# Performance work log

Hardware: AMD Instinct MI355X
Metric: run time of the kernel (lower is better)

Reference implementation:

```python
import jax, jax.numpy as jnp
import numpy as np

IN_FEATURES = 128
OUT_FEATURES = 1
N_NODES = 100000
N_EDGES = 640000


def setup_inputs() -> dict:
    key = jax.random.key(0)
    k1, k2, k3, k4, k5 = jax.random.split(key, 5)
    inp = jax.random.normal(k1, (N_NODES, IN_FEATURES), dtype=jnp.float32)
    edge_src = jax.random.randint(k2, (N_EDGES,), 0, N_NODES, dtype=jnp.int64)
    edge_trg = jax.random.randint(k3, (N_EDGES,), 0, N_NODES, dtype=jnp.int64)
    # Linear(2*in_features, out_features) with xavier_uniform weight init
    fan_in, fan_out = 2 * IN_FEATURES, OUT_FEATURES
    limit = float(np.sqrt(6.0 / (fan_in + fan_out)))
    W = jax.random.uniform(k4, (OUT_FEATURES, 2 * IN_FEATURES), dtype=jnp.float32,
                           minval=-limit, maxval=limit)
    b_lim = 1.0 / float(np.sqrt(fan_in))
    b = jax.random.uniform(k5, (OUT_FEATURES,), dtype=jnp.float32,
                           minval=-b_lim, maxval=b_lim)
    return {"input": inp, "edge_src_nodes": edge_src, "edge_trg_nodes": edge_trg,
            "W": W, "b": b}


def reference(input, W, b, edge_src_nodes, edge_trg_nodes):
    x = input.reshape(-1, input.shape[-1])          # [N, d]
    src = x[edge_src_nodes]                         # [E, d] gather
    trg = x[edge_trg_nodes]                         # [E, d] gather
    # Linear on concat(src, trg) == src @ W_src^T + trg @ W_trg^T (avoids concat materialization)
    d = x.shape[-1]
    W_src, W_trg = W[:, :d], W[:, d:]
    logits = src @ W_src.T + trg @ W_trg.T + b      # [E, out_features]
    return jax.nn.sigmoid(logits)
```

## Files before the change

### kernel.cpp

```cpp
#include <hip/hip_runtime.h>
#include <hip/hip_bf16.h>

#define N_FEAT 128

__global__ __launch_bounds__(256) void project_kernel(
    const float* __restrict__ x, const float* __restrict__ W,
    float* __restrict__ p_src, float* __restrict__ p_trg, int n_nodes)
{
    int gid  = blockIdx.x * blockDim.x + threadIdx.x;
    int node = gid >> 5;
    int sub  = threadIdx.x & 31;
    if (node >= n_nodes) return;

    const float4 xv = *reinterpret_cast<const float4*>(x + (size_t)node * N_FEAT + 4 * sub);
    const float4 ws = *reinterpret_cast<const float4*>(W + 4 * sub);
    const float4 wt = *reinterpret_cast<const float4*>(W + N_FEAT + 4 * sub);

    float ssrc = fmaf(xv.x, ws.x, fmaf(xv.y, ws.y, fmaf(xv.z, ws.z, xv.w * ws.w)));
    float strg = fmaf(xv.x, wt.x, fmaf(xv.y, wt.y, fmaf(xv.z, wt.z, xv.w * wt.w)));

    #pragma unroll
    for (int off = 16; off > 0; off >>= 1) {
        ssrc += __shfl_down(ssrc, off, 32);
        strg += __shfl_down(strg, off, 32);
    }
    if (sub == 0) {
        p_src[node] = ssrc;
        p_trg[node] = strg;
    }
}

__global__ __launch_bounds__(256) void edge_kernel(
    const int* __restrict__ esrc, const int* __restrict__ etrg,
    const float* __restrict__ p_src, const float* __restrict__ p_trg,
    const float* __restrict__ b, float* __restrict__ out, int n_edges4)
{
    int i = blockIdx.x * blockDim.x + threadIdx.x;
    if (i >= n_edges4) return;
    const int4 s = reinterpret_cast<const int4*>(esrc)[i];
    const int4 t = reinterpret_cast<const int4*>(etrg)[i];
    const float bias = b[0];

    float4 o;
    o.x = 1.0f / (1.0f + __expf(-(p_src[s.x] + p_trg[t.x] + bias)));
    o.y = 1.0f / (1.0f + __expf(-(p_src[s.y] + p_trg[t.y] + bias)));
    o.z = 1.0f / (1.0f + __expf(-(p_src[s.z] + p_trg[t.z] + bias)));
    o.w = 1.0f / (1.0f + __expf(-(p_src[s.w] + p_trg[t.w] + bias)));
    reinterpret_cast<float4*>(out)[i] = o;
}

extern "C" void kernel_launch(void* const* d_in, const int* in_sizes, int n_in,
                              void* d_out, int out_size, void* d_ws, size_t ws_size,
                              hipStream_t stream)
{
    const float* x    = (const float*)d_in[0];
    const int*   esrc = (const int*)d_in[1];
    const int*   etrg = (const int*)d_in[2];
    const float* W    = (const float*)d_in[3];
    const float* b    = (const float*)d_in[4];
    float* out = (float*)d_out;

    int n_nodes = in_sizes[0] / N_FEAT;
    int n_edges = in_sizes[1];

    float* p_src = (float*)d_ws;
    float* p_trg = p_src + n_nodes;

    const int threads = 256;
    int blocks1 = (n_nodes * 32 + threads - 1) / threads;
    project_kernel<<<blocks1, threads, 0, stream>>>(x, W, p_src, p_trg, n_nodes);

    int n_edges4 = n_edges / 4;
    int blocks2 = (n_edges4 + threads - 1) / threads;
    edge_kernel<<<blocks2, threads, 0, stream>>>(esrc, etrg, p_src, p_trg, b, out, n_edges4);
}
```

Measured before the change: 99.08 us.

## Fuse projection and edge kernels into one cooperative persistent kernel

Merges the node projection and the edge sigmoid into one persistent kernel with grid-stride loops, separated by a cooperative grid-wide sync. The goal is to save one kernel launch and the gap between the two dependent kernels. In exchange it pays for a grid barrier and the cooperative launch path. The grid is fixed at 1024 blocks, which may leave the GPU under-occupied for the memory-bound node pass.

Result: slower. 255.0 us (+157.4%).

```diff
diff --git a/kernel.cpp b/kernel.cpp
--- a/kernel.cpp
+++ b/kernel.cpp
@@ -1,52 +1,59 @@
 #include <hip/hip_runtime.h>
 #include <hip/hip_bf16.h>
+#include <hip/hip_cooperative_groups.h>
+
+namespace cg = cooperative_groups;
 
 #define N_FEAT 128
 
-__global__ __launch_bounds__(256) void project_kernel(
+__global__ __launch_bounds__(256, 4) void fused_kernel(
     const float* __restrict__ x, const float* __restrict__ W,
-    float* __restrict__ p_src, float* __restrict__ p_trg, int n_nodes)
+    const int* __restrict__ esrc, const int* __restrict__ etrg,
+    const float* __restrict__ b, float* __restrict__ out,
+    float* __restrict__ p_src, float* __restrict__ p_trg,
+    int n_nodes, int n_edges4)
 {
-    int gid  = blockIdx.x * blockDim.x + threadIdx.x;
-    int node = gid >> 5;
-    int sub  = threadIdx.x & 31;
-    if (node >= n_nodes) return;
+    cg::grid_group grid = cg::this_grid();
 
-    const float4 xv = *reinterpret_cast<const float4*>(x + (size_t)node * N_FEAT + 4 * sub);
+    const int nthreads = gridDim.x * blockDim.x;
+    const int nsegs = nthreads >> 5;
+    const int seg   = (blockIdx.x * blockDim.x + threadIdx.x) >> 5;
+    const int sub   = threadIdx.x & 31;
+
     const float4 ws = *reinterpret_cast<const float4*>(W + 4 * sub);
     const float4 wt = *reinterpret_cast<const float4*>(W + N_FEAT + 4 * sub);
 
-    float ssrc = fmaf(xv.x, ws.x, fmaf(xv.y, ws.y, fmaf(xv.z, ws.z, xv.w * ws.w)));
-    float strg = fmaf(xv.x, wt.x, fmaf(xv.y, wt.y, fmaf(xv.z, wt.z, xv.w * wt.w)));
+    for (int node = seg; node < n_nodes; node += nsegs) {
+        const float4 xv = *reinterpret_cast<const float4*>(
+            x + (size_t)node * N_FEAT + 4 * sub);
+        float ssrc = fmaf(xv.x, ws.x, fmaf(xv.y, ws.y, fmaf(xv.z, ws.z, xv.w * ws.w)));
+        float strg = fmaf(xv.x, wt.x, fmaf(xv.y, wt.y, fmaf(xv.z, wt.z, xv.w * wt.w)));
+        #pragma unroll
+        for (int off = 16; off > 0; off >>= 1) {
+            ssrc += __shfl_down(ssrc, off, 32);
+            strg += __shfl_down(strg, off, 32);
+        }
+        if (sub == 0) {
+            p_src[node] = ssrc;
+            p_trg[node] = strg;
+        }
+    }
 
-    #pragma unroll
-    for (int off = 16; off > 0; off >>= 1) {
-        ssrc += __shfl_down(ssrc, off, 32);
-        strg += __shfl_down(strg, off, 32);
+    __threadfence();
+    grid.sync();
+
+    const int tid  = blockIdx.x * blockDim.x + threadIdx.x;
+    const float bias = b[0];
+    for (int i = tid; i < n_edges4; i += nthreads) {
+        const int4 s = reinterpret_cast<const int4*>(esrc)[i];
+        const int4 t = reinterpret_cast<const int4*>(etrg)[i];
+        float4 o;
+        o.x = 1.0f / (1.0f + __expf(-(p_src[s.x] + p_trg[t.x] + bias)));
+        o.y = 1.0f / (1.0f + __expf(-(p_src[s.y] + p_trg[t.y] + bias)));
+        o.z = 1.0f / (1.0f + __expf(-(p_src[s.z] + p_trg[t.z] + bias)));
+        o.w = 1.0f / (1.0f + __expf(-(p_src[s.w] + p_trg[t.w] + bias)));
+        reinterpret_cast<float4*>(out)[i] = o;
     }
-    if (sub == 0) {
-        p_src[node] = ssrc;
-        p_trg[node] = strg;
-    }
-}
-
-__global__ __launch_bounds__(256) void edge_kernel(
-    const int* __restrict__ esrc, const int* __restrict__ etrg,
-    const float* __restrict__ p_src, const float* __restrict__ p_trg,
-    const float* __restrict__ b, float* __restrict__ out, int n_edges4)
-{
-    int i = blockIdx.x * blockDim.x + threadIdx.x;
-    if (i >= n_edges4) return;
-    const int4 s = reinterpret_cast<const int4*>(esrc)[i];
-    const int4 t = reinterpret_cast<const int4*>(etrg)[i];
-    const float bias = b[0];
-
-    float4 o;
-    o.x = 1.0f / (1.0f + __expf(-(p_src[s.x] + p_trg[t.x] + bias)));
-    o.y = 1.0f / (1.0f + __expf(-(p_src[s.y] + p_trg[t.y] + bias)));
-    o.z = 1.0f / (1.0f + __expf(-(p_src[s.z] + p_trg[t.z] + bias)));
-    o.w = 1.0f / (1.0f + __expf(-(p_src[s.w] + p_trg[t.w] + bias)));
-    reinterpret_cast<float4*>(out)[i] = o;
 }
 
 extern "C" void kernel_launch(void* const* d_in, const int* in_sizes, int n_in,
@@ -60,17 +67,17 @@
     const float* b    = (const float*)d_in[4];
     float* out = (float*)d_out;
 
-    int n_nodes = in_sizes[0] / N_FEAT;
-    int n_edges = in_sizes[1];
+    int n_nodes  = in_sizes[0] / N_FEAT;
+    int n_edges  = in_sizes[1];
+    int n_edges4 = n_edges / 4;
 
     float* p_src = (float*)d_ws;
     float* p_trg = p_src + n_nodes;
 
-    const int threads = 256;
-    int blocks1 = (n_nodes * 32 + threads - 1) / threads;
-    project_kernel<<<blocks1, threads, 0, stream>>>(x, W, p_src, p_trg, n_nodes);
-
-    int n_edges4 = n_edges / 4;
-    int blocks2 = (n_edges4 + threads - 1) / threads;
-    edge_kernel<<<blocks2, threads, 0, stream>>>(esrc, etrg, p_src, p_trg, b, out, n_edges4);
+    dim3 grid(1024), block(256);
+    void* args[] = { (void*)&x, (void*)&W, (void*)&esrc, (void*)&etrg,
+                     (void*)&b, (void*)&out, (void*)&p_src, (void*)&p_trg,
+                     (void*)&n_nodes, (void*)&n_edges4 };
+    hipLaunchCooperativeKernel((const void*)fused_kernel, grid, block,
+                               args, 0, stream);
 }
```
